# Optimization experiments

Hardware: AMD Instinct MI355X
Metric: run time of the kernel (lower is better)

## Reference

```python
import jax, jax.numpy as jnp
import numpy as np
import math

TAU = 1.0  # init kwarg tau


def setup_inputs() -> dict:
    key = jax.random.key(0)
    n, m = 1024, 8192
    V = jax.random.normal(key, (n, m), dtype=jnp.float32)
    return {"V": V}


def reference(V) -> jnp.ndarray:
    n, m = V.shape
    num_rounds = math.ceil(m / n)
    # Repeat V row-blocks num_rounds times: M has shape [num_rounds*n, m]
    M = jnp.tile(V, (num_rounds, 1))

    def step(c, row):
        # Soft round-robin pick (training branch of SoftRR.__one_round)
        y = jax.nn.softmax((row - jnp.min(row) + 1.0) * c / TAU)
        c = (1.0 - y) * c
        return c, y

    c0 = jnp.ones((m,), dtype=V.dtype)
    _, R = jax.lax.scan(step, c0, M)  # R: [num_rounds*n, m]
    pi = R.reshape(num_rounds, n, m).sum(axis=0)  # [n, m]
    return pi
```

## Files before the change

kernel.cpp:

```cpp
#include <hip/hip_runtime.h>
#include <hip/hip_fp16.h>


#define N_ROWS 1024
#define M_COLS 8192
#define STEPS  8192
#define LOG2E  1.4426950408889634f

using half8  = __attribute__((ext_vector_type(8))) _Float16;
using half2v = __attribute__((ext_vector_type(2))) _Float16;

__device__ __forceinline__ float fast_exp2(float x) {
#if __has_builtin(__builtin_amdgcn_exp2f)
  return __builtin_amdgcn_exp2f(x);
#else
  return exp2f(x);
#endif
}
__device__ __forceinline__ float fast_rcp(float x) {
#if __has_builtin(__builtin_amdgcn_rcpf)
  return __builtin_amdgcn_rcpf(x);
#else
  return 1.0f / x;
#endif
}
__device__ __forceinline__ unsigned pack_f16_u32(float y0, float y1) {
  return __builtin_bit_cast(unsigned, __builtin_amdgcn_cvt_pkrtz(y0, y1));
}

template <int CTRL>
__device__ __forceinline__ float dpp_add(float x) {
  int yi = __builtin_amdgcn_update_dpp(0, __builtin_bit_cast(int, x),
                                       CTRL, 0xf, 0xf, true);
  return x + __builtin_bit_cast(float, yi);
}

__device__ __forceinline__ float wave_sum_to_lane63(float x) {
  x = dpp_add<0x111>(x);
  x = dpp_add<0x112>(x);
  x = dpp_add<0x114>(x);
  x = dpp_add<0x118>(x);
  x = dpp_add<0x142>(x);
  x = dpp_add<0x143>(x);
  return x;
}

__global__ void softrr_rowmin(const float* __restrict__ V, float* __restrict__ rmin) {
  const int row = blockIdx.x;
  const float* p = V + (size_t)row * M_COLS;
  float m = 1e30f;
  for (int j = threadIdx.x; j < M_COLS; j += 256) m = fminf(m, p[j]);
#pragma unroll
  for (int off = 32; off; off >>= 1) m = fminf(m, __shfl_xor(m, off, 64));
  __shared__ float sm[4];
  if ((threadIdx.x & 63) == 0) sm[threadIdx.x >> 6] = m;
  __syncthreads();
  if (threadIdx.x == 0) {
    rmin[row] = fminf(fminf(sm[0], sm[1]), fminf(sm[2], sm[3]));
  }
}

__global__ void softrr_prep16(const float* __restrict__ V, const float* __restrict__ rmin,
                              __half* __restrict__ A) {
  const int idx8 = blockIdx.x * 256 + threadIdx.x;
  const int row = idx8 >> 10;
  const float mn = rmin[row];
  const float4* v4 = (const float4*)V;
  float4 va = v4[2 * idx8];
  float4 vb = v4[2 * idx8 + 1];
  half8 o;
  o[0] = (_Float16)((va.x - mn + 1.0f) * LOG2E);
  o[1] = (_Float16)((va.y - mn + 1.0f) * LOG2E);
  o[2] = (_Float16)((va.z - mn + 1.0f) * LOG2E);
  o[3] = (_Float16)((va.w - mn + 1.0f) * LOG2E);
  o[4] = (_Float16)((vb.x - mn + 1.0f) * LOG2E);
  o[5] = (_Float16)((vb.y - mn + 1.0f) * LOG2E);
  o[6] = (_Float16)((vb.z - mn + 1.0f) * LOG2E);
  o[7] = (_Float16)((vb.w - mn + 1.0f) * LOG2E);
  ((half8*)A)[idx8] = o;
}

template <int POS>
__device__ __forceinline__ void rr_step_df(
    int s,
    const half8& acur, half8& adst,
    float (&e)[8], float (&c)[8], uint4& o,
    const half8* __restrict__ A8, uint4* __restrict__ R4,
    unsigned long long (*ring)[16], int t, int lane, int wavei)
{
  R4[(size_t)((s - 1) & (STEPS - 1)) * 1024 + t] = o;
  adst = A8[((s + 3) & (N_ROWS - 1)) * 1024 + t];

  const unsigned want = (unsigned)(s + 1);
  unsigned long long v;
  do {
    v = __hip_atomic_load(&ring[POS][lane & 15], __ATOMIC_RELAXED,
                          __HIP_MEMORY_SCOPE_WORKGROUP);
  } while ((unsigned)(v >> 32) != want);
  float x = __uint_as_float((unsigned)v);

  x = dpp_add<0x111>(x);
  x = dpp_add<0x112>(x);
  x = dpp_add<0x114>(x);
  x = dpp_add<0x118>(x);
  const float S = __builtin_bit_cast(
      float, __builtin_amdgcn_readlane(__builtin_bit_cast(int, x), 15));
  const float Sinv = fast_rcp(S);

  float y[8];
#pragma unroll
  for (int k = 0; k < 8; ++k) {
    y[k] = e[k] * Sinv;
    c[k] = __builtin_fmaf(-y[k], c[k], c[k]);
    e[k] = fast_exp2(__builtin_fmaf((float)acur[k], c[k], 0.0f));
  }
  float l = ((e[0] + e[1]) + (e[2] + e[3])) + ((e[4] + e[5]) + (e[6] + e[7]));
  l = wave_sum_to_lane63(l);
  if (lane == 63) {
    const unsigned long long pv =
        ((unsigned long long)(unsigned)(s + 2) << 32) |
        (unsigned long long)__builtin_bit_cast(unsigned, l);
    __hip_atomic_store(&ring[(POS + 1) & 3][wavei], pv, __ATOMIC_RELAXED,
                       __HIP_MEMORY_SCOPE_WORKGROUP);
  }

  o.x = pack_f16_u32(y[0], y[1]);
  o.y = pack_f16_u32(y[2], y[3]);
  o.z = pack_f16_u32(y[4], y[5]);
  o.w = pack_f16_u32(y[6], y[7]);
}

__global__ void __launch_bounds__(1024) softrr_scan_df(const __half* __restrict__ Ah,
                                                       __half* __restrict__ Rh) {
  const int t = threadIdx.x;
  const int wavei = t >> 6;
  const int lane = t & 63;
  __shared__ unsigned long long ring[4][16];

  const half8* __restrict__ A8 = (const half8*)Ah;
  uint4* __restrict__ R4 = (uint4*)Rh;

  if (t < 64) ring[t >> 4][t & 15] = 0ULL;
  __syncthreads();

  float c[8], e[8];
#pragma unroll
  for (int k = 0; k < 8; ++k) c[k] = 1.0f;

  half8 r0 = A8[t];
  half8 pA = A8[1024 + t];
  half8 pB = A8[2048 + t];
  half8 pC, pD;

#pragma unroll
  for (int k = 0; k < 8; ++k) e[k] = fast_exp2((float)r0[k]);
  {
    float l = ((e[0] + e[1]) + (e[2] + e[3])) + ((e[4] + e[5]) + (e[6] + e[7]));
    l = wave_sum_to_lane63(l);
    if (lane == 63) {
      const unsigned long long pv =
          (1ULL << 32) | (unsigned long long)__builtin_bit_cast(unsigned, l);
      __hip_atomic_store(&ring[0][wavei], pv, __ATOMIC_RELAXED,
                         __HIP_MEMORY_SCOPE_WORKGROUP);
    }
  }
  uint4 o = make_uint4(0u, 0u, 0u, 0u);

  for (int s = 0; s < STEPS; s += 4) {
    rr_step_df<0>(s + 0, pA, pC, e, c, o, A8, R4, ring, t, lane, wavei);
    rr_step_df<1>(s + 1, pB, pD, e, c, o, A8, R4, ring, t, lane, wavei);
    rr_step_df<2>(s + 2, pC, pA, e, c, o, A8, R4, ring, t, lane, wavei);
    rr_step_df<3>(s + 3, pD, pB, e, c, o, A8, R4, ring, t, lane, wavei);
  }

  R4[(size_t)(STEPS - 1) * 1024 + t] = o;
}

__global__ void softrr_sum8(const __half* __restrict__ Rh, float* __restrict__ out) {
  const int idx8 = blockIdx.x * 256 + threadIdx.x;
  const half8* R8 = (const half8*)Rh;
  float acc[8];
  {
    half8 v = R8[idx8];
#pragma unroll
    for (int k = 0; k < 8; ++k) acc[k] = (float)v[k];
  }
#pragma unroll
  for (int r = 1; r < 8; ++r) {
    half8 v = R8[(size_t)r * 1024 * 1024 + idx8];
#pragma unroll
    for (int k = 0; k < 8; ++k) acc[k] += (float)v[k];
  }
  ((float4*)out)[2 * idx8]     = make_float4(acc[0], acc[1], acc[2], acc[3]);
  ((float4*)out)[2 * idx8 + 1] = make_float4(acc[4], acc[5], acc[6], acc[7]);
}

__global__ void __launch_bounds__(1024) softrr_scan_b(const float* __restrict__ V,
                                                      const float* __restrict__ rmin,
                                                      float* __restrict__ out) {
  const int t = threadIdx.x;
  const int wave = t >> 6;
  const int lane = t & 63;
  __shared__ float partials[2][16];
  __shared__ float smin[N_ROWS];
  smin[t] = rmin[t];
  __syncthreads();
  const float4* __restrict__ V4 = (const float4*)V;
  float4* O4 = (float4*)out;
  float c[8];
#pragma unroll
  for (int k = 0; k < 8; ++k) c[k] = 1.0f;
  float4 va = V4[2 * t], vb = V4[2 * t + 1];
  float4 pa, pb;
  for (int s = 0; s < STEPS; ++s) {
    const int i = s & (N_ROWS - 1);
    const int r = s >> 10;
    const int in_ = (s + 1) & (N_ROWS - 1);
    float4 van = V4[in_ * 2048 + 2 * t];
    float4 vbn = V4[in_ * 2048 + 2 * t + 1];
    const float mn = smin[i];
    const float base = (1.0f - mn) * LOG2E;
    float vv[8] = {va.x, va.y, va.z, va.w, vb.x, vb.y, vb.z, vb.w};
    float e[8];
    float l = 0.0f;
#pragma unroll
    for (int k = 0; k < 8; ++k) {
      float zb = __builtin_fmaf(vv[k], LOG2E, base);
      e[k] = fast_exp2(zb * c[k]);
      l += e[k];
    }
#pragma unroll
    for (int off = 32; off; off >>= 1) l += __shfl_xor(l, off, 64);
    if (lane == 0) partials[s & 1][wave] = l;
    __syncthreads();
    float S = 0.0f;
#pragma unroll
    for (int w = 0; w < 16; ++w) S += partials[s & 1][w];
    const float Sinv = fast_rcp(S);
    float po[8] = {pa.x, pa.y, pa.z, pa.w, pb.x, pb.y, pb.z, pb.w};
    float o[8];
#pragma unroll
    for (int k = 0; k < 8; ++k) {
      float y = e[k] * Sinv;
      c[k] = __builtin_fmaf(-y, c[k], c[k]);
      o[k] = (r > 0) ? (po[k] + y) : y;
    }
    O4[i * 2048 + 2 * t]     = make_float4(o[0], o[1], o[2], o[3]);
    O4[i * 2048 + 2 * t + 1] = make_float4(o[4], o[5], o[6], o[7]);
    va = van; vb = vbn;
    pa = O4[in_ * 2048 + 2 * t];
    pb = O4[in_ * 2048 + 2 * t + 1];
  }
}

extern "C" void kernel_launch(void* const* d_in, const int* in_sizes, int n_in,
                              void* d_out, int out_size, void* d_ws, size_t ws_size,
                              hipStream_t stream) {
  const float* V = (const float*)d_in[0];
  float* out = (float*)d_out;
  float* rmin = (float*)d_ws;

  const size_t A16_BYTES = (size_t)N_ROWS * M_COLS * 2;
  const size_t R_BYTES   = (size_t)STEPS * M_COLS * 2;
  const size_t need_df   = 4096 + A16_BYTES + R_BYTES;

  if (ws_size >= need_df) {
    __half* A = (__half*)((char*)d_ws + 4096);
    __half* R = (__half*)((char*)d_ws + 4096 + A16_BYTES);
    softrr_rowmin<<<N_ROWS, 256, 0, stream>>>(V, rmin);
    softrr_prep16<<<4096, 256, 0, stream>>>(V, rmin, A);
    softrr_scan_df<<<1, 1024, 0, stream>>>(A, R);
    softrr_sum8<<<4096, 256, 0, stream>>>(R, out);
  } else {
    softrr_rowmin<<<N_ROWS, 256, 0, stream>>>(V, rmin);
    softrr_scan_b<<<1, 1024, 0, stream>>>(V, rmin, out);
  }
}
```

Measured before the change: 4.436 ms.

## Split sequential scan across 16 workgroups with global-memory ring synchronization

The single 1024-thread workgroup scan is replaced by 16 workgroups of 256 threads, each thread handling 2 columns instead of 8. Per-wave partial sums of the softmax denominator now pass through an agent-scope ring buffer in global memory, which is zeroed inside the prep kernel. The aim is to cut the per-step serial arithmetic per thread and spread the work over more compute units. In exchange, every step needs a cross-CU handshake through L2 with higher latency, and the scheme depends on all 16 blocks being resident at once.

```diff
diff --git a/kernel.cpp b/kernel.cpp
--- a/kernel.cpp
+++ b/kernel.cpp
@@ -6,6 +6,8 @@
 #define M_COLS 8192
 #define STEPS  8192
 #define LOG2E  1.4426950408889634f
+#define NBLK   16
+#define TPB_MC 256
 
 using half8  = __attribute__((ext_vector_type(8))) _Float16;
 using half2v = __attribute__((ext_vector_type(2))) _Float16;
@@ -61,7 +63,10 @@
 }
 
 __global__ void softrr_prep16(const float* __restrict__ V, const float* __restrict__ rmin,
-                              __half* __restrict__ A) {
+                              __half* __restrict__ A,
+                              unsigned long long* __restrict__ ringz) {
+  if (blockIdx.x == 0 && threadIdx.x < 256) ringz[threadIdx.x] = 0ULL;
+
   const int idx8 = blockIdx.x * 256 + threadIdx.x;
   const int row = idx8 >> 10;
   const float mn = rmin[row];
@@ -81,99 +86,94 @@
 }
 
 template <int POS>
-__device__ __forceinline__ void rr_step_df(
-    int s,
-    const half8& acur, half8& adst,
-    float (&e)[8], float (&c)[8], uint4& o,
-    const half8* __restrict__ A8, uint4* __restrict__ R4,
-    unsigned long long (*ring)[16], int t, int lane, int wavei)
+__device__ __forceinline__ void rr_step_mc(
+    int s, const unsigned acur, unsigned& adst,
+    float& e0, float& e1, float& c0, float& c1, unsigned& o,
+    const unsigned* __restrict__ A2, unsigned* __restrict__ R2,
+    unsigned long long (*__restrict__ ring)[64], int cp, int lane, int slot)
 {
-  R4[(size_t)((s - 1) & (STEPS - 1)) * 1024 + t] = o;
-  adst = A8[((s + 3) & (N_ROWS - 1)) * 1024 + t];
+  R2[(size_t)((s - 1) & (STEPS - 1)) * 4096 + cp] = o;
+  adst = A2[((s + 3) & (N_ROWS - 1)) * 4096 + cp];
 
   const unsigned want = (unsigned)(s + 1);
   unsigned long long v;
   do {
-    v = __hip_atomic_load(&ring[POS][lane & 15], __ATOMIC_RELAXED,
-                          __HIP_MEMORY_SCOPE_WORKGROUP);
-  } while ((unsigned)(v >> 32) != want);
+    v = __hip_atomic_load(&ring[POS][lane], __ATOMIC_RELAXED,
+                          __HIP_MEMORY_SCOPE_AGENT);
+  } while (__any((unsigned)(v >> 32) != want));
   float x = __uint_as_float((unsigned)v);
 
-  x = dpp_add<0x111>(x);
-  x = dpp_add<0x112>(x);
-  x = dpp_add<0x114>(x);
-  x = dpp_add<0x118>(x);
+  x = wave_sum_to_lane63(x);
   const float S = __builtin_bit_cast(
-      float, __builtin_amdgcn_readlane(__builtin_bit_cast(int, x), 15));
+      float, __builtin_amdgcn_readlane(__builtin_bit_cast(int, x), 63));
   const float Sinv = fast_rcp(S);
 
-  float y[8];
-#pragma unroll
-  for (int k = 0; k < 8; ++k) {
-    y[k] = e[k] * Sinv;
-    c[k] = __builtin_fmaf(-y[k], c[k], c[k]);
-    e[k] = fast_exp2(__builtin_fmaf((float)acur[k], c[k], 0.0f));
-  }
-  float l = ((e[0] + e[1]) + (e[2] + e[3])) + ((e[4] + e[5]) + (e[6] + e[7]));
+  const half2v a2 = __builtin_bit_cast(half2v, acur);
+  const float y0 = e0 * Sinv;
+  const float y1 = e1 * Sinv;
+  c0 = __builtin_fmaf(-y0, c0, c0);
+  c1 = __builtin_fmaf(-y1, c1, c1);
+  e0 = fast_exp2(__builtin_fmaf((float)a2[0], c0, 0.0f));
+  e1 = fast_exp2(__builtin_fmaf((float)a2[1], c1, 0.0f));
+  float l = e0 + e1;
   l = wave_sum_to_lane63(l);
   if (lane == 63) {
     const unsigned long long pv =
         ((unsigned long long)(unsigned)(s + 2) << 32) |
         (unsigned long long)__builtin_bit_cast(unsigned, l);
-    __hip_atomic_store(&ring[(POS + 1) & 3][wavei], pv, __ATOMIC_RELAXED,
-                       __HIP_MEMORY_SCOPE_WORKGROUP);
-  }
-
-  o.x = pack_f16_u32(y[0], y[1]);
-  o.y = pack_f16_u32(y[2], y[3]);
-  o.z = pack_f16_u32(y[4], y[5]);
-  o.w = pack_f16_u32(y[6], y[7]);
-}
-
-__global__ void __launch_bounds__(1024) softrr_scan_df(const __half* __restrict__ Ah,
-                                                       __half* __restrict__ Rh) {
+    __hip_atomic_store(&ring[(POS + 1) & 3][slot], pv, __ATOMIC_RELAXED,
+                       __HIP_MEMORY_SCOPE_AGENT);
+  }
+
+  o = pack_f16_u32(y0, y1);
+}
+
+__global__ void __launch_bounds__(TPB_MC) softrr_scan_mc(
+    const __half* __restrict__ Ah, __half* __restrict__ Rh,
+    unsigned long long* __restrict__ ringp) {
+  const int b = blockIdx.x;
   const int t = threadIdx.x;
   const int wavei = t >> 6;
   const int lane = t & 63;
-  __shared__ unsigned long long ring[4][16];
-
-  const half8* __restrict__ A8 = (const half8*)Ah;
-  uint4* __restrict__ R4 = (uint4*)Rh;
-
-  if (t < 64) ring[t >> 4][t & 15] = 0ULL;
-  __syncthreads();
-
-  float c[8], e[8];
-#pragma unroll
-  for (int k = 0; k < 8; ++k) c[k] = 1.0f;
-
-  half8 r0 = A8[t];
-  half8 pA = A8[1024 + t];
-  half8 pB = A8[2048 + t];
-  half8 pC, pD;
-
-#pragma unroll
-  for (int k = 0; k < 8; ++k) e[k] = fast_exp2((float)r0[k]);
+  const int slot = (b << 2) | wavei;
+  const int cp = b * 256 + t;
+
+  unsigned long long (*__restrict__ ring)[64] =
+      (unsigned long long (*)[64])ringp;
+  const unsigned* __restrict__ A2 = (const unsigned*)Ah;
+  unsigned* __restrict__ R2 = (unsigned*)Rh;
+
+  float c0 = 1.0f, c1 = 1.0f;
+
+  const unsigned r0 = A2[cp];
+  unsigned pA = A2[4096 + cp];
+  unsigned pB = 0; pB = A2[2 * 4096 + cp];
+  unsigned pC, pD;
+
+  float e0, e1;
   {
-    float l = ((e[0] + e[1]) + (e[2] + e[3])) + ((e[4] + e[5]) + (e[6] + e[7]));
+    const half2v a2 = __builtin_bit_cast(half2v, r0);
+    e0 = fast_exp2((float)a2[0]);
+    e1 = fast_exp2((float)a2[1]);
+    float l = e0 + e1;
     l = wave_sum_to_lane63(l);
     if (lane == 63) {
       const unsigned long long pv =
           (1ULL << 32) | (unsigned long long)__builtin_bit_cast(unsigned, l);
-      __hip_atomic_store(&ring[0][wavei], pv, __ATOMIC_RELAXED,
-                         __HIP_MEMORY_SCOPE_WORKGROUP);
+      __hip_atomic_store(&ring[0][slot], pv, __ATOMIC_RELAXED,
+                         __HIP_MEMORY_SCOPE_AGENT);
     }
   }
-  uint4 o = make_uint4(0u, 0u, 0u, 0u);
+  unsigned o = 0u;
 
   for (int s = 0; s < STEPS; s += 4) {
-    rr_step_df<0>(s + 0, pA, pC, e, c, o, A8, R4, ring, t, lane, wavei);
-    rr_step_df<1>(s + 1, pB, pD, e, c, o, A8, R4, ring, t, lane, wavei);
-    rr_step_df<2>(s + 2, pC, pA, e, c, o, A8, R4, ring, t, lane, wavei);
-    rr_step_df<3>(s + 3, pD, pB, e, c, o, A8, R4, ring, t, lane, wavei);
-  }
-
-  R4[(size_t)(STEPS - 1) * 1024 + t] = o;
+    rr_step_mc<0>(s + 0, pA, pC, e0, e1, c0, c1, o, A2, R2, ring, cp, lane, slot);
+    rr_step_mc<1>(s + 1, pB, pD, e0, e1, c0, c1, o, A2, R2, ring, cp, lane, slot);
+    rr_step_mc<2>(s + 2, pC, pA, e0, e1, c0, c1, o, A2, R2, ring, cp, lane, slot);
+    rr_step_mc<3>(s + 3, pD, pB, e0, e1, c0, c1, o, A2, R2, ring, cp, lane, slot);
+  }
+
+  R2[(size_t)(STEPS - 1) * 4096 + cp] = o;
 }
 
 __global__ void softrr_sum8(const __half* __restrict__ Rh, float* __restrict__ out) {
@@ -260,16 +260,19 @@
   float* out = (float*)d_out;
   float* rmin = (float*)d_ws;
 
-  const size_t A16_BYTES = (size_t)N_ROWS * M_COLS * 2;
-  const size_t R_BYTES   = (size_t)STEPS * M_COLS * 2;
-  const size_t need_df   = 4096 + A16_BYTES + R_BYTES;
-
-  if (ws_size >= need_df) {
-    __half* A = (__half*)((char*)d_ws + 4096);
-    __half* R = (__half*)((char*)d_ws + 4096 + A16_BYTES);
+  const size_t RING_OFF = 4096;
+  const size_t A_OFF    = 8192;
+  const size_t A_BYTES  = (size_t)N_ROWS * M_COLS * 2;
+  const size_t R_BYTES  = (size_t)STEPS * M_COLS * 2;
+  const size_t need_mc  = A_OFF + A_BYTES + R_BYTES;
+
+  if (ws_size >= need_mc) {
+    unsigned long long* ring = (unsigned long long*)((char*)d_ws + RING_OFF);
+    __half* A = (__half*)((char*)d_ws + A_OFF);
+    __half* R = (__half*)((char*)d_ws + A_OFF + A_BYTES);
     softrr_rowmin<<<N_ROWS, 256, 0, stream>>>(V, rmin);
-    softrr_prep16<<<4096, 256, 0, stream>>>(V, rmin, A);
-    softrr_scan_df<<<1, 1024, 0, stream>>>(A, R);
+    softrr_prep16<<<4096, 256, 0, stream>>>(V, rmin, A, ring);
+    softrr_scan_mc<<<NBLK, TPB_MC, 0, stream>>>(A, R, ring);
     softrr_sum8<<<4096, 256, 0, stream>>>(R, out);
   } else {
     softrr_rowmin<<<N_ROWS, 256, 0, stream>>>(V, rmin);
```

Measured after the change: 15.37 ms. 246% more time.

## Replace spin-polled LDS ring with double-buffered partials and s_barrier per step

Applied to the files above, without the earlier changes.

Per-step cross-wave softmax denominator exchange switches from tagged 64-bit atomic ring slots polled in a spin loop to a double-buffered float array in LDS synchronized by a raw s_waitcnt lgkmcnt(0) + s_barrier. This removes the polling loop and tag packing, and lets outstanding global loads/stores stay in flight across the barrier. It trades the decoupled per-wave progress of the ring for a full workgroup barrier every step.

```diff
diff --git a/kernel.cpp b/kernel.cpp
--- a/kernel.cpp
+++ b/kernel.cpp
@@ -24,8 +24,8 @@
   return 1.0f / x;
 #endif
 }
-__device__ __forceinline__ unsigned pack_f16_u32(float y0, float y1) {
-  return __builtin_bit_cast(unsigned, __builtin_amdgcn_cvt_pkrtz(y0, y1));
+__device__ __forceinline__ half2v pack_f16(float y0, float y1) {
+  return __builtin_bit_cast(half2v, __builtin_amdgcn_cvt_pkrtz(y0, y1));
 }
 
 template <int CTRL>
@@ -44,6 +44,8 @@
   x = dpp_add<0x143>(x);
   return x;
 }
+
+#define BAR_LDS_ONLY() asm volatile("s_waitcnt lgkmcnt(0)\n\ts_barrier" ::: "memory")
 
 __global__ void softrr_rowmin(const float* __restrict__ V, float* __restrict__ rmin) {
   const int row = blockIdx.x;
@@ -80,24 +82,19 @@
   ((half8*)A)[idx8] = o;
 }
 
-template <int POS>
-__device__ __forceinline__ void rr_step_df(
+__device__ __forceinline__ void rr_step16(
     int s,
     const half8& acur, half8& adst,
-    float (&e)[8], float (&c)[8], uint4& o,
-    const half8* __restrict__ A8, uint4* __restrict__ R4,
-    unsigned long long (*ring)[16], int t, int lane, int wavei)
+    float (&e)[8], float (&c)[8], half8& o,
+    const half8* __restrict__ A8, half8* __restrict__ R8,
+    float (*sP)[16], int t, int lane, int wave)
 {
-  R4[(size_t)((s - 1) & (STEPS - 1)) * 1024 + t] = o;
+  const int par = s & 1;
+  float x = (lane < 16) ? sP[par][lane] : 0.0f;
+
+  R8[(size_t)((s - 1) & (STEPS - 1)) * 1024 + t] = o;
+
   adst = A8[((s + 3) & (N_ROWS - 1)) * 1024 + t];
-
-  const unsigned want = (unsigned)(s + 1);
-  unsigned long long v;
-  do {
-    v = __hip_atomic_load(&ring[POS][lane & 15], __ATOMIC_RELAXED,
-                          __HIP_MEMORY_SCOPE_WORKGROUP);
-  } while ((unsigned)(v >> 32) != want);
-  float x = __uint_as_float((unsigned)v);
 
   x = dpp_add<0x111>(x);
   x = dpp_add<0x112>(x);
@@ -116,32 +113,28 @@
   }
   float l = ((e[0] + e[1]) + (e[2] + e[3])) + ((e[4] + e[5]) + (e[6] + e[7]));
   l = wave_sum_to_lane63(l);
-  if (lane == 63) {
-    const unsigned long long pv =
-        ((unsigned long long)(unsigned)(s + 2) << 32) |
-        (unsigned long long)__builtin_bit_cast(unsigned, l);
-    __hip_atomic_store(&ring[(POS + 1) & 3][wavei], pv, __ATOMIC_RELAXED,
-                       __HIP_MEMORY_SCOPE_WORKGROUP);
-  }
-
-  o.x = pack_f16_u32(y[0], y[1]);
-  o.y = pack_f16_u32(y[2], y[3]);
-  o.z = pack_f16_u32(y[4], y[5]);
-  o.w = pack_f16_u32(y[6], y[7]);
-}
-
-__global__ void __launch_bounds__(1024) softrr_scan_df(const __half* __restrict__ Ah,
-                                                       __half* __restrict__ Rh) {
+  if (lane == 63) sP[par ^ 1][wave] = l;
+
+  {
+    half2v h0 = pack_f16(y[0], y[1]);
+    half2v h1 = pack_f16(y[2], y[3]);
+    half2v h2 = pack_f16(y[4], y[5]);
+    half2v h3 = pack_f16(y[6], y[7]);
+    o[0] = h0[0]; o[1] = h0[1]; o[2] = h1[0]; o[3] = h1[1];
+    o[4] = h2[0]; o[5] = h2[1]; o[6] = h3[0]; o[7] = h3[1];
+  }
+  BAR_LDS_ONLY();
+}
+
+__global__ void __launch_bounds__(1024) softrr_scan_nor(const __half* __restrict__ Ah,
+                                                        __half* __restrict__ Rh) {
   const int t = threadIdx.x;
-  const int wavei = t >> 6;
+  const int wave = t >> 6;
   const int lane = t & 63;
-  __shared__ unsigned long long ring[4][16];
+  __shared__ float sP[2][16];
 
   const half8* __restrict__ A8 = (const half8*)Ah;
-  uint4* __restrict__ R4 = (uint4*)Rh;
-
-  if (t < 64) ring[t >> 4][t & 15] = 0ULL;
-  __syncthreads();
+  half8* __restrict__ R8 = (half8*)Rh;
 
   float c[8], e[8];
 #pragma unroll
@@ -157,23 +150,24 @@
   {
     float l = ((e[0] + e[1]) + (e[2] + e[3])) + ((e[4] + e[5]) + (e[6] + e[7]));
     l = wave_sum_to_lane63(l);
-    if (lane == 63) {
-      const unsigned long long pv =
-          (1ULL << 32) | (unsigned long long)__builtin_bit_cast(unsigned, l);
-      __hip_atomic_store(&ring[0][wavei], pv, __ATOMIC_RELAXED,
-                         __HIP_MEMORY_SCOPE_WORKGROUP);
-    }
-  }
-  uint4 o = make_uint4(0u, 0u, 0u, 0u);
+    if (lane == 63) sP[0][wave] = l;
+  }
+  half8 o;
+  {
+    half2v z = pack_f16(0.0f, 0.0f);
+    o[0]=z[0]; o[1]=z[1]; o[2]=z[0]; o[3]=z[1];
+    o[4]=z[0]; o[5]=z[1]; o[6]=z[0]; o[7]=z[1];
+  }
+  BAR_LDS_ONLY();
 
   for (int s = 0; s < STEPS; s += 4) {
-    rr_step_df<0>(s + 0, pA, pC, e, c, o, A8, R4, ring, t, lane, wavei);
-    rr_step_df<1>(s + 1, pB, pD, e, c, o, A8, R4, ring, t, lane, wavei);
-    rr_step_df<2>(s + 2, pC, pA, e, c, o, A8, R4, ring, t, lane, wavei);
-    rr_step_df<3>(s + 3, pD, pB, e, c, o, A8, R4, ring, t, lane, wavei);
-  }
-
-  R4[(size_t)(STEPS - 1) * 1024 + t] = o;
+    rr_step16(s + 0, pA, pC, e, c, o, A8, R8, sP, t, lane, wave);
+    rr_step16(s + 1, pB, pD, e, c, o, A8, R8, sP, t, lane, wave);
+    rr_step16(s + 2, pC, pA, e, c, o, A8, R8, sP, t, lane, wave);
+    rr_step16(s + 3, pD, pB, e, c, o, A8, R8, sP, t, lane, wave);
+  }
+
+  R8[(size_t)(STEPS - 1) * 1024 + t] = o;
 }
 
 __global__ void softrr_sum8(const __half* __restrict__ Rh, float* __restrict__ out) {
@@ -260,16 +254,16 @@
   float* out = (float*)d_out;
   float* rmin = (float*)d_ws;
 
-  const size_t A16_BYTES = (size_t)N_ROWS * M_COLS * 2;
-  const size_t R_BYTES   = (size_t)STEPS * M_COLS * 2;
-  const size_t need_df   = 4096 + A16_BYTES + R_BYTES;
-
-  if (ws_size >= need_df) {
+  const size_t A_BYTES = (size_t)N_ROWS * M_COLS * 2;
+  const size_t R_BYTES = (size_t)STEPS * M_COLS * 2;
+  const size_t need_nor = 4096 + A_BYTES + R_BYTES;
+
+  if (ws_size >= need_nor) {
     __half* A = (__half*)((char*)d_ws + 4096);
-    __half* R = (__half*)((char*)d_ws + 4096 + A16_BYTES);
+    __half* R = (__half*)((char*)d_ws + 4096 + A_BYTES);
     softrr_rowmin<<<N_ROWS, 256, 0, stream>>>(V, rmin);
     softrr_prep16<<<4096, 256, 0, stream>>>(V, rmin, A);
-    softrr_scan_df<<<1, 1024, 0, stream>>>(A, R);
+    softrr_scan_nor<<<1, 1024, 0, stream>>>(A, R);
     softrr_sum8<<<4096, 256, 0, stream>>>(R, out);
   } else {
     softrr_rowmin<<<N_ROWS, 256, 0, stream>>>(V, rmin);
```

Measured after the change: 4.282 ms. 1.04x faster.
